# Kernel tuning notes

Hardware: AMD Instinct MI355X
Metric: run time of the kernel (lower is better)

## Reference

```python
import jax, jax.numpy as jnp
import numpy as np

DIM, HEADS = 1024, 16
HD = DIM // HEADS  # head_dim = 64
EPS = 1e-5


def setup_inputs() -> dict:
    key = jax.random.key(0)
    ks = jax.random.split(key, 8)
    B, N = 2, 2048
    x = jax.random.normal(ks[0], (B, N, DIM), dtype=jnp.float32)
    # RoPE table: [N, HD//2, 2] = (cos, sin) per position/freq
    inv_freq = 1.0 / (10000.0 ** (jnp.arange(0, HD, 2, dtype=jnp.float32) / HD))  # [HD//2]
    angles = jnp.arange(N, dtype=jnp.float32)[:, None] * inv_freq[None, :]        # [N, HD//2]
    freq_cis = jnp.stack([jnp.cos(angles), jnp.sin(angles)], axis=-1)             # [N, HD//2, 2]
    s = 0.02
    Wqkv = jax.random.normal(ks[1], (DIM, 3 * DIM), dtype=jnp.float32) * s
    ln_q_g = jnp.ones((HD,), jnp.float32)
    ln_q_b = jnp.zeros((HD,), jnp.float32)
    ln_k_g = jnp.ones((HD,), jnp.float32)
    ln_k_b = jnp.zeros((HD,), jnp.float32)
    Wproj = jax.random.normal(ks[2], (DIM, DIM), dtype=jnp.float32) * s
    bproj = jnp.zeros((DIM,), jnp.float32)
    return {"x": x, "freq_cis": freq_cis, "Wqkv": Wqkv,
            "ln_q_g": ln_q_g, "ln_q_b": ln_q_b, "ln_k_g": ln_k_g, "ln_k_b": ln_k_b,
            "Wproj": Wproj, "bproj": bproj}


def _layernorm(t, g, b):
    mu = jnp.mean(t, axis=-1, keepdims=True)
    var = jnp.mean(jnp.square(t - mu), axis=-1, keepdims=True)
    return (t - mu) * jax.lax.rsqrt(var + EPS) * g + b


def _rope(t, cos, sin):
    # t: [b, n, h, hd]; pairs are interleaved (even=real, odd=imag)
    b, n, h, hd = t.shape
    tr = jnp.transpose(t[..., 0::2], (0, 2, 1, 3))  # [b, h, n, hd//2]
    ti = jnp.transpose(t[..., 1::2], (0, 2, 1, 3))
    out_r = tr * cos - ti * sin
    out_i = tr * sin + ti * cos
    return jnp.stack([out_r, out_i], axis=-1).reshape(b, h, n, hd)  # [b, h, n, hd]


def reference(x, freq_cis, Wqkv, ln_q_g, ln_q_b, ln_k_g, ln_k_b, Wproj, bproj):
    B, N, _ = x.shape
    qkv = (x @ Wqkv).reshape(B, N, 3, HEADS, HD)  # split is outermost in the packed dim
    q, k, v = qkv[:, :, 0], qkv[:, :, 1], qkv[:, :, 2]  # [b, n, h, hd]
    q = _layernorm(q, ln_q_g, ln_q_b)
    k = _layernorm(k, ln_k_g, ln_k_b)
    cos = freq_cis[None, None, :, :, 0]  # [1, 1, n, hd//2]
    sin = freq_cis[None, None, :, :, 1]
    q = _rope(q, cos, sin)  # [b, h, n, hd]
    k = _rope(k, cos, sin)
    v = jnp.transpose(v, (0, 2, 1, 3))  # [b, h, n, hd]
    scores = jnp.einsum('bhqd,bhkd->bhqk', q, k) * (1.0 / np.sqrt(HD))
    attn = jax.nn.softmax(scores, axis=-1)
    out = jnp.einsum('bhqk,bhkd->bhqd', attn, v)
    out = jnp.transpose(out, (0, 2, 1, 3)).reshape(B, N, HEADS * HD)
    return out @ Wproj + bproj
```

## Files before the change

kernel.cpp:

```cpp
#include <hip/hip_runtime.h>

typedef __bf16 bf16_t;
typedef bf16_t bf16x8 __attribute__((ext_vector_type(8)));
typedef bf16_t bf16x4 __attribute__((ext_vector_type(4)));
typedef float f32x4 __attribute__((ext_vector_type(4)));
typedef short s16x4 __attribute__((ext_vector_type(4)));

typedef __attribute__((address_space(1))) void* as1_void;
typedef __attribute__((address_space(3))) void* as3_void;

static constexpr int kDim   = 1024;
static constexpr int kHeads = 16;
static constexpr int kHd    = 64;
static constexpr int kBatch = 2;
static constexpr int kSeq   = 2048;
static constexpr int kM     = kBatch * kSeq;
static constexpr int kNqkv  = 3 * kDim;
static constexpr float kQScale = 0.125f * 1.4426950408889634f;
static constexpr float kFixedMax = 16.0f;

__device__ __forceinline__ void gld_lds16(const bf16_t* g, bf16_t* l) {
  __builtin_amdgcn_global_load_lds((as1_void)(void*)const_cast<bf16_t*>(g),
                                   (as3_void)(void*)l, 16, 0, 0);
}

__device__ __forceinline__ f32x4 mfma16(s16x4 a, s16x4 b, f32x4 c) {
#if __has_builtin(__builtin_amdgcn_mfma_f32_16x16x16bf16_1k)
  return __builtin_amdgcn_mfma_f32_16x16x16bf16_1k(a, b, c, 0, 0, 0);
#else
  f32x4 d;
  asm volatile("v_mfma_f32_16x16x16_bf16 %0, %1, %2, %3"
               : "=v"(d) : "v"(a), "v"(b), "v"(c));
  return d;
#endif
}

__device__ __forceinline__ unsigned pack2_bf16(float lo, float hi) {
  unsigned a = __builtin_bit_cast(unsigned, lo) + 0x8000u;
  unsigned b = __builtin_bit_cast(unsigned, hi) + 0x8000u;
  return __builtin_amdgcn_perm(b, a, 0x07060302u);
}

__global__ __launch_bounds__(256) void prep(const float* __restrict__ x, bf16_t* __restrict__ xb,
                                            const float* __restrict__ Wqkv, bf16_t* __restrict__ WqkvT,
                                            const float* __restrict__ Wproj, bf16_t* __restrict__ WprojT) {
  __shared__ float tile[32][33];
  const int bid = blockIdx.x, tid = threadIdx.x;
  if (bid < 1024) {
#pragma unroll
    for (int j = 0; j < 4; ++j) {
      const int i = bid * 1024 + j * 256 + tid;
      const float4 f = ((const float4*)x)[i];
      bf16x4 o;
      o[0] = (bf16_t)f.x; o[1] = (bf16_t)f.y; o[2] = (bf16_t)f.z; o[3] = (bf16_t)f.w;
      ((bf16x4*)xb)[i] = o;
    }
    return;
  }
  const float* in; bf16_t* out; int R, C, t;
  if (bid < 4096) { in = Wqkv;  out = WqkvT;  R = kDim; C = kNqkv; t = bid - 1024; }
  else            { in = Wproj; out = WprojT; R = kDim; C = kDim;  t = bid - 4096; }
  const int ntx = C / 32;
  const int c0 = (t % ntx) * 32, r0 = (t / ntx) * 32;
  const int tx = tid & 31, ty = tid >> 5;
#pragma unroll
  for (int j = 0; j < 4; ++j)
    tile[ty + 8 * j][tx] = in[(size_t)(r0 + ty + 8 * j) * C + (c0 + tx)];
  __syncthreads();
#pragma unroll
  for (int j = 0; j < 4; ++j)
    out[(size_t)(c0 + ty + 8 * j) * R + (r0 + tx)] = (bf16_t)tile[tx][ty + 8 * j];
}

__global__ __launch_bounds__(256) void gemm_proj_64(const bf16_t* __restrict__ A,
                                                    const bf16_t* __restrict__ Bt,
                                                    float* __restrict__ Cout,
                                                    const float* __restrict__ bias) {
  const int N = kDim, K = kDim;
  __shared__ __align__(16) bf16_t lA[64 * 32];
  __shared__ __align__(16) bf16_t lB[128 * 32];
  const int tid  = threadIdx.x;
  const int w    = tid >> 6, lane = tid & 63;
  const int quad = lane >> 4, l16 = lane & 15;
  const int m0 = blockIdx.y * 64, n0 = blockIdx.x * 128;

  const int strow = tid >> 2;
  const int stcol = (tid & 3) * 8;
  const bf16_t* gA = A  + (size_t)(m0 + strow) * K + stcol;
  const bf16_t* gB = Bt + (size_t)(n0 + strow) * K + stcol;
  bf16_t* lA0 = lA + w * 512;
  bf16_t* lB0 = lB + w * 512;
  bf16_t* lB1 = lB + 2048 + w * 512;

  f32x4 acc[4][2];
#pragma unroll
  for (int i = 0; i < 4; ++i)
#pragma unroll
    for (int j = 0; j < 2; ++j)
#pragma unroll
      for (int r = 0; r < 4; ++r) acc[i][j][r] = 0.f;

  for (int kb = 0; kb < (K >> 5); ++kb) {
    const int k0 = kb * 32;
    __syncthreads();
    gld_lds16(gA + k0, lA0);
    gld_lds16(gB + k0, lB0);
    gld_lds16(gB + (size_t)64 * K + k0, lB1);
    __syncthreads();
    bf16x8 af[4], bfr[2];
#pragma unroll
    for (int mt = 0; mt < 4; ++mt)
      af[mt] = *(const bf16x8*)(lA + (mt * 16 + l16) * 32 + quad * 8);
#pragma unroll
    for (int nt = 0; nt < 2; ++nt)
      bfr[nt] = *(const bf16x8*)(lB + (w * 32 + nt * 16 + l16) * 32 + quad * 8);
#pragma unroll
    for (int mt = 0; mt < 4; ++mt)
#pragma unroll
      for (int nt = 0; nt < 2; ++nt)
        acc[mt][nt] = __builtin_amdgcn_mfma_f32_16x16x32_bf16(af[mt], bfr[nt], acc[mt][nt], 0, 0, 0);
  }

#pragma unroll
  for (int mt = 0; mt < 4; ++mt)
#pragma unroll
    for (int nt = 0; nt < 2; ++nt)
#pragma unroll
      for (int r = 0; r < 4; ++r) {
        const int row = m0 + mt * 16 + quad * 4 + r;
        const int col = n0 + w * 32 + nt * 16 + l16;
        Cout[(size_t)row * N + col] = acc[mt][nt][r] + bias[col];
      }
}

__global__ __launch_bounds__(256) void gemm_qkv_fused(
    const bf16_t* __restrict__ A, const bf16_t* __restrict__ Bt,
    const float* __restrict__ freq,
    const float* __restrict__ gq, const float* __restrict__ bq,
    const float* __restrict__ gk, const float* __restrict__ bk,
    bf16_t* __restrict__ Q, bf16_t* __restrict__ Kout, bf16_t* __restrict__ Vt) {
  __shared__ __align__(16) char smem[34816];
  bf16_t* lA = (bf16_t*)smem;
  bf16_t* lB = lA + 128 * 32;
  const int tid  = threadIdx.x;
  const int w    = tid >> 6, lane = tid & 63;
  const int quad = lane >> 4, l16 = lane & 15;
  const int wm = w >> 1, wn = w & 1;
  const int m0 = blockIdx.y * 128, n0 = blockIdx.x * 128;
  const int K = kDim;

  const int strow = tid >> 2;
  const int stcol = (tid & 3) * 8;
  const bf16_t* gA = A  + (size_t)(m0 + strow) * K + stcol;
  const bf16_t* gB = Bt + (size_t)(n0 + strow) * K + stcol;
  bf16_t* lA0 = lA + w * 512;
  bf16_t* lA1 = lA + 2048 + w * 512;
  bf16_t* lB0 = lB + w * 512;
  bf16_t* lB1 = lB + 2048 + w * 512;

  f32x4 acc[4][4];
#pragma unroll
  for (int i = 0; i < 4; ++i)
#pragma unroll
    for (int j = 0; j < 4; ++j)
#pragma unroll
      for (int r = 0; r < 4; ++r) acc[i][j][r] = 0.f;

  for (int kb = 0; kb < (K >> 5); ++kb) {
    const int k0 = kb * 32;
    __syncthreads();
    gld_lds16(gA + k0, lA0);
    gld_lds16(gA + (size_t)64 * K + k0, lA1);
    gld_lds16(gB + k0, lB0);
    gld_lds16(gB + (size_t)64 * K + k0, lB1);
    __syncthreads();
    bf16x8 af[4], bfr[4];
#pragma unroll
    for (int mt = 0; mt < 4; ++mt)
      af[mt] = *(const bf16x8*)(lA + (wm * 64 + mt * 16 + l16) * 32 + quad * 8);
#pragma unroll
    for (int nt = 0; nt < 4; ++nt)
      bfr[nt] = *(const bf16x8*)(lB + (wn * 64 + nt * 16 + l16) * 32 + quad * 8);
#pragma unroll
    for (int mt = 0; mt < 4; ++mt)
#pragma unroll
      for (int nt = 0; nt < 4; ++nt)
        acc[mt][nt] = __builtin_amdgcn_mfma_f32_16x16x32_bf16(af[mt], bfr[nt], acc[mt][nt], 0, 0, 0);
  }

  const int mat = n0 >> 10;
  const int cin = (n0 & 1023) + wn * 64;
  const int h   = cin >> 6;
  const int bb  = m0 >> 11;
  const int bh  = bb * kHeads + h;
  const int nrow0 = (m0 & 2047) + wm * 64;

  if (mat == 2) {
#pragma unroll
    for (int mt = 0; mt < 4; ++mt)
#pragma unroll
      for (int nt = 0; nt < 4; ++nt) {
        bf16x4 pk;
#pragma unroll
        for (int r = 0; r < 4; ++r) pk[r] = (bf16_t)acc[mt][nt][r];
        const int d = nt * 16 + l16;
        *(bf16x4*)(Vt + ((size_t)bh * kHd + d) * kSeq + nrow0 + mt * 16 + quad * 4) = pk;
      }
    return;
  }

  __syncthreads();
  float* fsm = (float*)smem;
  {
    const int row = tid >> 1, half = tid & 1;
    const float4* src = (const float4*)(freq + ((size_t)(m0 & 2047) + row) * 64 + half * 32);
    float4* dst4 = (float4*)(fsm + row * 68 + half * 32);
#pragma unroll
    for (int j = 0; j < 8; ++j) dst4[j] = src[j];
  }
  __syncthreads();

  const float* gv_ = (mat == 0) ? gq : gk;
  const float* bv_ = (mat == 0) ? bq : bk;
  float gv[4], bv[4];
#pragma unroll
  for (int nt = 0; nt < 4; ++nt) { gv[nt] = gv_[nt * 16 + l16]; bv[nt] = bv_[nt * 16 + l16]; }
  bf16_t* dst = (mat == 0) ? Q : Kout;
  const float sgn = (l16 & 1) ? 1.f : -1.f;
  const float scl = (mat == 0) ? kQScale : 1.f;

#pragma unroll
  for (int mt = 0; mt < 4; ++mt) {
    float mu[4], inv[4];
#pragma unroll
    for (int r = 0; r < 4; ++r) {
      float s = acc[mt][0][r] + acc[mt][1][r] + acc[mt][2][r] + acc[mt][3][r];
      s += __shfl_xor(s, 1); s += __shfl_xor(s, 2);
      s += __shfl_xor(s, 4); s += __shfl_xor(s, 8);
      mu[r] = s * (1.f / 64.f);
    }
#pragma unroll
    for (int r = 0; r < 4; ++r) {
      float vs = 0.f;
#pragma unroll
      for (int nt = 0; nt < 4; ++nt) {
        const float dd = acc[mt][nt][r] - mu[r];
        vs += dd * dd;
      }
      vs += __shfl_xor(vs, 1); vs += __shfl_xor(vs, 2);
      vs += __shfl_xor(vs, 4); vs += __shfl_xor(vs, 8);
      inv[r] = rsqrtf(vs * (1.f / 64.f) + 1e-5f);
    }
#pragma unroll
    for (int nt = 0; nt < 4; ++nt) {
#pragma unroll
      for (int r = 0; r < 4; ++r) {
        const float y = (acc[mt][nt][r] - mu[r]) * inv[r] * gv[nt] + bv[nt];
        const float part = __shfl_xor(y, 1);
        const int mloc = wm * 64 + mt * 16 + quad * 4 + r;
        const float2 cs = *(const float2*)(fsm + mloc * 68 + ((nt * 16 + l16) & ~1));
        const float outv = (y * cs.x + sgn * part * cs.y) * scl;
        dst[((size_t)bh * kSeq + nrow0 + mt * 16 + quad * 4 + r) * kHd + nt * 16 + l16] =
            (bf16_t)outv;
      }
    }
  }
}

__global__ __launch_bounds__(256) void flash_attn9(const bf16_t* __restrict__ Q,
                                                   const bf16_t* __restrict__ K,
                                                   const bf16_t* __restrict__ Vt,
                                                   bf16_t* __restrict__ O) {
  __shared__ __align__(16) bf16_t lK[2][64 * 72];
  __shared__ __align__(16) bf16_t lV[2][64 * 72];
  const int tid  = threadIdx.x;
  const int w    = tid >> 6, lane = tid & 63;
  const int quad = lane >> 4, l16 = lane & 15;
  const int bh = blockIdx.x & 31;
  const int qb = blockIdx.x >> 5;
  const int b = bh >> 4, h = bh & 15;
  const int q0 = qb * 128 + w * 32;
  const bf16_t* Qb = Q  + (size_t)bh * kSeq * kHd;
  const bf16_t* Kb = K  + (size_t)bh * kSeq * kHd;
  const bf16_t* Vb = Vt + (size_t)bh * kHd * kSeq;

  bf16x8 qf[2][2];
#pragma unroll
  for (int nt = 0; nt < 2; ++nt)
#pragma unroll
    for (int ks = 0; ks < 2; ++ks)
      qf[nt][ks] = *(const bf16x8*)(Qb + (size_t)(q0 + nt * 16 + l16) * kHd + ks * 32 + quad * 8);

  s16x4 onesA;
#pragma unroll
  for (int j = 0; j < 4; ++j) onesA[j] = (l16 == 0) ? (short)0x3F80 : (short)0;

  const int srow = tid >> 2;
  const int scol = (tid & 3) * 16;

  bf16x8 kreg[2], vreg[2];
#pragma unroll
  for (int p = 0; p < 2; ++p) {
    kreg[p] = *(const bf16x8*)(Kb + (size_t)srow * kHd + scol + 8 * p);
    vreg[p] = *(const bf16x8*)(Vb + (size_t)srow * kSeq + scol + 8 * p);
  }
#pragma unroll
  for (int p = 0; p < 2; ++p) {
    *(bf16x8*)(&lK[0][srow * 72 + scol + 8 * p]) = kreg[p];
    *(bf16x8*)(&lV[0][srow * 72 + scol + 8 * p]) = vreg[p];
  }
#pragma unroll
  for (int p = 0; p < 2; ++p) {
    kreg[p] = *(const bf16x8*)(Kb + (size_t)(64 + srow) * kHd + scol + 8 * p);
    vreg[p] = *(const bf16x8*)(Vb + (size_t)srow * kSeq + 64 + scol + 8 * p);
  }
  __syncthreads();

  f32x4 o[4][2];
  f32x4 osum[2];
#pragma unroll
  for (int nt = 0; nt < 2; ++nt) {
#pragma unroll
    for (int r = 0; r < 4; ++r) osum[nt][r] = 0.f;
#pragma unroll
    for (int ntd = 0; ntd < 4; ++ntd)
#pragma unroll
      for (int r = 0; r < 4; ++r) o[ntd][nt][r] = 0.f;
  }

  const int nIter = kSeq / 64;

  for (int it = 0; it < nIter; ++it) {
    const int cur = it & 1;
    if (it + 1 < nIter) {
#pragma unroll
      for (int p = 0; p < 2; ++p) {
        *(bf16x8*)(&lK[cur ^ 1][srow * 72 + scol + 8 * p]) = kreg[p];
        *(bf16x8*)(&lV[cur ^ 1][srow * 72 + scol + 8 * p]) = vreg[p];
      }
      if (it + 2 < nIter) {
        const int kvn = (it + 2) * 64;
#pragma unroll
        for (int p = 0; p < 2; ++p) {
          kreg[p] = *(const bf16x8*)(Kb + (size_t)(kvn + srow) * kHd + scol + 8 * p);
          vreg[p] = *(const bf16x8*)(Vb + (size_t)srow * kSeq + kvn + scol + 8 * p);
        }
      }
    }

    f32x4 st[4][2];
#pragma unroll
    for (int mt = 0; mt < 4; ++mt)
#pragma unroll
      for (int nt = 0; nt < 2; ++nt)
#pragma unroll
        for (int r = 0; r < 4; ++r) st[mt][nt][r] = -kFixedMax;
#pragma unroll
    for (int ks = 0; ks < 2; ++ks) {
      bf16x8 kf[4];
#pragma unroll
      for (int mt = 0; mt < 4; ++mt)
        kf[mt] = *(const bf16x8*)(&lK[cur][(mt * 16 + l16) * 72 + ks * 32 + quad * 8]);
#pragma unroll
      for (int mt = 0; mt < 4; ++mt)
#pragma unroll
        for (int nt = 0; nt < 2; ++nt)
          st[mt][nt] = __builtin_amdgcn_mfma_f32_16x16x32_bf16(kf[mt], qf[nt][ks], st[mt][nt], 0, 0, 0);
    }

    s16x4 pb[4][2];
#pragma unroll
    for (int mt = 0; mt < 4; ++mt)
#pragma unroll
      for (int nt = 0; nt < 2; ++nt) {
        float e0 = exp2f(st[mt][nt][0]);
        float e1 = exp2f(st[mt][nt][1]);
        float e2 = exp2f(st[mt][nt][2]);
        float e3 = exp2f(st[mt][nt][3]);
        uint2 u;
        u.x = pack2_bf16(e0, e1);
        u.y = pack2_bf16(e2, e3);
        pb[mt][nt] = __builtin_bit_cast(s16x4, u);
      }

#pragma unroll
    for (int mt = 0; mt < 4; ++mt) {
#pragma unroll
      for (int ntd = 0; ntd < 4; ++ntd) {
        const s16x4 va = *(const s16x4*)(&lV[cur][(ntd * 16 + l16) * 72 + mt * 16 + quad * 4]);
#pragma unroll
        for (int nt = 0; nt < 2; ++nt)
          o[ntd][nt] = mfma16(va, pb[mt][nt], o[ntd][nt]);
      }
#pragma unroll
      for (int nt = 0; nt < 2; ++nt)
        osum[nt] = mfma16(onesA, pb[mt][nt], osum[nt]);
    }
    __syncthreads();
  }

#pragma unroll
  for (int nt = 0; nt < 2; ++nt) {
    const float rl = __shfl(osum[nt][0], l16);
    const float inv = 1.f / rl;
    const int row = q0 + nt * 16 + l16;
#pragma unroll
    for (int ntd = 0; ntd < 4; ++ntd) {
      bf16x4 ov;
#pragma unroll
      for (int r = 0; r < 4; ++r) ov[r] = (bf16_t)(o[ntd][nt][r] * inv);
      *(bf16x4*)(O + ((size_t)(b * kSeq + row)) * kDim + h * kHd + ntd * 16 + quad * 4) = ov;
    }
  }
}

extern "C" void kernel_launch(void* const* d_in, const int* in_sizes, int n_in,
                              void* d_out, int out_size, void* d_ws, size_t ws_size,
                              hipStream_t stream) {
  const float* x     = (const float*)d_in[0];
  const float* freq  = (const float*)d_in[1];
  const float* Wqkv  = (const float*)d_in[2];
  const float* gq    = (const float*)d_in[3];
  const float* bq    = (const float*)d_in[4];
  const float* gk    = (const float*)d_in[5];
  const float* bk    = (const float*)d_in[6];
  const float* Wproj = (const float*)d_in[7];
  const float* bproj = (const float*)d_in[8];
  float* out = (float*)d_out;

  char* ws = (char*)d_ws;
  bf16_t* xb     = (bf16_t*)(ws + 0);
  bf16_t* WqkvT  = (bf16_t*)(ws + 8388608);
  bf16_t* WprojT = (bf16_t*)(ws + 14680064);
  bf16_t* Qb     = (bf16_t*)(ws + 16777216);
  bf16_t* Kb     = (bf16_t*)(ws + 25165824);
  bf16_t* Vtb    = (bf16_t*)(ws + 33554432);
  bf16_t* obuf   = (bf16_t*)(ws + 41943040);

  prep<<<dim3(5120), dim3(256), 0, stream>>>(x, xb, Wqkv, WqkvT, Wproj, WprojT);
  gemm_qkv_fused<<<dim3(kNqkv / 128, kM / 128), dim3(256), 0, stream>>>(
      xb, WqkvT, freq, gq, bq, gk, bk, Qb, Kb, Vtb);
  flash_attn9<<<dim3((kSeq / 128) * kBatch * kHeads), dim3(256), 0, stream>>>(Qb, Kb, Vtb, obuf);
  gemm_proj_64<<<dim3(kDim / 128, kM / 64), dim3(256), 0, stream>>>(obuf, WprojT, out, bproj);
}
```

Before: 227.6 us.

## Split attention across two KV halves and merge partials in a combine kernel

Flash attention now splits each head's KV sequence into two halves, doubling the grid. Each half writes unnormalized bf16 partial outputs and per-row softmax sums. A new combine kernel adds the partials and divides by the summed row totals before the projection GEMM. This relies on the fixed-max softmax so partials add directly, and it aims to raise parallelism and latency hiding. The cost is an extra kernel launch, extra memory traffic, and rounding the unnormalized partials to bf16.

```diff
diff --git a/kernel.cpp b/kernel.cpp
--- a/kernel.cpp
+++ b/kernel.cpp
@@ -267,22 +267,27 @@
   }
 }
 
-__global__ __launch_bounds__(256) void flash_attn9(const bf16_t* __restrict__ Q,
-                                                   const bf16_t* __restrict__ K,
-                                                   const bf16_t* __restrict__ Vt,
-                                                   bf16_t* __restrict__ O) {
+__global__ __launch_bounds__(256) void flash_attn11(const bf16_t* __restrict__ Q,
+                                                    const bf16_t* __restrict__ K,
+                                                    const bf16_t* __restrict__ Vt,
+                                                    bf16_t* __restrict__ Op0,
+                                                    bf16_t* __restrict__ Op1,
+                                                    float* __restrict__ rsum) {
   __shared__ __align__(16) bf16_t lK[2][64 * 72];
   __shared__ __align__(16) bf16_t lV[2][64 * 72];
   const int tid  = threadIdx.x;
   const int w    = tid >> 6, lane = tid & 63;
   const int quad = lane >> 4, l16 = lane & 15;
   const int bh = blockIdx.x & 31;
-  const int qb = blockIdx.x >> 5;
+  const int t2 = blockIdx.x >> 5;
+  const int qb = t2 & 15;
+  const int sp = t2 >> 4;
   const int b = bh >> 4, h = bh & 15;
   const int q0 = qb * 128 + w * 32;
+  const int kv0 = sp * (kSeq / 2);
   const bf16_t* Qb = Q  + (size_t)bh * kSeq * kHd;
-  const bf16_t* Kb = K  + (size_t)bh * kSeq * kHd;
-  const bf16_t* Vb = Vt + (size_t)bh * kHd * kSeq;
+  const bf16_t* Kb = K  + (size_t)bh * kSeq * kHd + (size_t)kv0 * kHd;
+  const bf16_t* Vb = Vt + (size_t)bh * kHd * kSeq + kv0;
 
   bf16x8 qf[2][2];
 #pragma unroll
@@ -328,7 +333,7 @@
       for (int r = 0; r < 4; ++r) o[ntd][nt][r] = 0.f;
   }
 
-  const int nIter = kSeq / 64;
+  const int nIter = kSeq / 128;
 
   for (int it = 0; it < nIter; ++it) {
     const int cur = it & 1;
@@ -399,19 +404,44 @@
     __syncthreads();
   }
 
+  if (quad == 0) {
+#pragma unroll
+    for (int nt = 0; nt < 2; ++nt)
+      rsum[((size_t)sp * 32 + bh) * kSeq + q0 + nt * 16 + l16] = osum[nt][0];
+  }
+
+  bf16_t* op = sp ? Op1 : Op0;
 #pragma unroll
   for (int nt = 0; nt < 2; ++nt) {
-    const float rl = __shfl(osum[nt][0], l16);
-    const float inv = 1.f / rl;
     const int row = q0 + nt * 16 + l16;
 #pragma unroll
     for (int ntd = 0; ntd < 4; ++ntd) {
       bf16x4 ov;
 #pragma unroll
-      for (int r = 0; r < 4; ++r) ov[r] = (bf16_t)(o[ntd][nt][r] * inv);
-      *(bf16x4*)(O + ((size_t)(b * kSeq + row)) * kDim + h * kHd + ntd * 16 + quad * 4) = ov;
-    }
-  }
+      for (int r = 0; r < 4; ++r) ov[r] = (bf16_t)o[ntd][nt][r];
+      *(bf16x4*)(op + ((size_t)(b * kSeq + row)) * kDim + h * kHd + ntd * 16 + quad * 4) = ov;
+    }
+  }
+}
+
+__global__ __launch_bounds__(256) void combine(bf16_t* __restrict__ p0,
+                                               const bf16_t* __restrict__ p1,
+                                               const float* __restrict__ rs) {
+  const int tid = threadIdx.x;
+  const int row = blockIdx.x * 2 + (tid >> 7);
+  const int col = (tid & 127) * 8;
+  const int h = col >> 6;
+  const int b = row >> 11;
+  const int r = row & 2047;
+  const int bh = b * kHeads + h;
+  const float inv = 1.f / (rs[(size_t)bh * kSeq + r] + rs[(size_t)(32 + bh) * kSeq + r]);
+  const size_t idx = (size_t)row * kDim + col;
+  const bf16x8 a = *(const bf16x8*)(p0 + idx);
+  const bf16x8 c = *(const bf16x8*)(p1 + idx);
+  bf16x8 o;
+#pragma unroll
+  for (int j = 0; j < 8; ++j) o[j] = (bf16_t)(((float)a[j] + (float)c[j]) * inv);
+  *(bf16x8*)(p0 + idx) = o;
 }
 
 extern "C" void kernel_launch(void* const* d_in, const int* in_sizes, int n_in,
@@ -435,11 +465,15 @@
   bf16_t* Qb     = (bf16_t*)(ws + 16777216);
   bf16_t* Kb     = (bf16_t*)(ws + 25165824);
   bf16_t* Vtb    = (bf16_t*)(ws + 33554432);
-  bf16_t* obuf   = (bf16_t*)(ws + 41943040);
+  bf16_t* part0  = (bf16_t*)(ws + 41943040);
+  bf16_t* part1  = (bf16_t*)(ws + 0);
+  float*  rsum   = (float*)(ws + 8388608);
 
   prep<<<dim3(5120), dim3(256), 0, stream>>>(x, xb, Wqkv, WqkvT, Wproj, WprojT);
   gemm_qkv_fused<<<dim3(kNqkv / 128, kM / 128), dim3(256), 0, stream>>>(
       xb, WqkvT, freq, gq, bq, gk, bk, Qb, Kb, Vtb);
-  flash_attn9<<<dim3((kSeq / 128) * kBatch * kHeads), dim3(256), 0, stream>>>(Qb, Kb, Vtb, obuf);
-  gemm_proj_64<<<dim3(kDim / 128, kM / 64), dim3(256), 0, stream>>>(obuf, WprojT, out, bproj);
-}
+  flash_attn11<<<dim3((kSeq / 128) * 2 * kBatch * kHeads), dim3(256), 0, stream>>>(
+      Qb, Kb, Vtb, part0, part1, rsum);
+  combine<<<dim3(kM / 2), dim3(256), 0, stream>>>(part0, part1, rsum);
+  gemm_proj_64<<<dim3(kDim / 128, kM / 64), dim3(256), 0, stream>>>(part0, WprojT, out, bproj);
+}
```

Measured after the change: 234.5 us. +3.1%, slower.
